# Kernel tuning notes

Hardware: AMD Instinct MI355X
Metric: run time of the kernel (lower is better)

The kernel has to match this reference:

```python
import jax, jax.numpy as jnp
import numpy as np

E, H, I, T, K = 8, 2048, 1024, 4096, 2
GROUP = 32


def dequant_int4(packed, scale, group):
    """packed: [E, R, C//2] ints in [0,256) holding two 4-bit values per byte.
    scale: [E, R, C//group]. Returns fp32 [E, R, C] with w = (nibble - 8) * scale."""
    lo = (packed & 0xF) - 8          # even columns
    hi = ((packed >> 4) & 0xF) - 8   # odd columns
    e, r, ch = packed.shape
    w = jnp.stack([lo, hi], axis=-1).reshape(e, r, 2 * ch).astype(jnp.float32)
    w = w.reshape(e, r, -1, group) * scale[..., None]
    return w.reshape(e, r, 2 * ch)


def setup_inputs() -> dict:
    key = jax.random.key(0)
    ks = jax.random.split(key, 6)
    x = jax.random.normal(ks[0], (T, H), dtype=jnp.float32)
    w1 = jax.random.randint(ks[1], (E, 2 * I, H // 2), 0, 256, dtype=jnp.int32)
    w1_scale = jax.random.uniform(ks[2], (E, 2 * I, H // GROUP), dtype=jnp.float32) * 0.02
    w2 = jax.random.randint(ks[3], (E, H, I // 2), 0, 256, dtype=jnp.int32)
    w2_scale = jax.random.uniform(ks[4], (E, H, I // GROUP), dtype=jnp.float32) * 0.02
    logits = jax.random.normal(ks[5], (T, E), dtype=jnp.float32)
    top_vals, top_idx = jax.lax.top_k(logits, K)
    expert_weights = jax.nn.softmax(top_vals, axis=-1)   # [T, K]
    expert_indices = top_idx.astype(jnp.int32)           # [T, K]
    return {"x": x, "w1": w1, "w1_scale": w1_scale, "w2": w2,
            "w2_scale": w2_scale, "expert_weights": expert_weights,
            "expert_indices": expert_indices, "top_k": K}


def reference(x, w1, w1_scale, w2, w2_scale, expert_weights, expert_indices, top_k):
    inter = w2.shape[2] * 2
    W1 = dequant_int4(w1, w1_scale, GROUP)   # [E, 2I, H]
    W2 = dequant_int4(w2, w2_scale, GROUP)   # [E, H, I]
    y13 = jnp.einsum('th,erh->etr', x, W1)   # [E, T, 2I]
    gate, up = y13[..., :inter], y13[..., inter:]
    h = jax.nn.silu(gate) * up               # [E, T, I] SwiGLU
    y = jnp.einsum('eti,ehi->eth', h, W2)    # [E, T, H]
    t_ids = jnp.arange(x.shape[0])[:, None]  # [T, 1]
    sel = y[expert_indices, t_ids, :]        # [T, K, H]
    return jnp.einsum('tkh,tk->th', sel, expert_weights)
```

## Files before the change

kernel.cpp:

```cpp
#include <hip/hip_runtime.h>
#include <cstdint>
#include <cstddef>

typedef unsigned int u32;
typedef unsigned short u16;
typedef __bf16 bf16x8 __attribute__((ext_vector_type(8)));
typedef float f32x4 __attribute__((ext_vector_type(4)));
typedef u16 u16x8 __attribute__((ext_vector_type(8)));

static constexpr int T_TOK = 4096;
static constexpr int HID   = 2048;
static constexpr int INTER = 1024;
static constexpr int NEXP  = 8;
static constexpr int TOPK  = 2;
static constexpr int SLOT_CAP = 10240;
static constexpr int NT_M = SLOT_CAP / 256;

static constexpr int META_TOK = 32;
static constexpr int META_SLOTOF = 32 + SLOT_CAP;

__device__ __forceinline__ u16 f2bf(float f) {
  u32 u = __builtin_bit_cast(u32, f);
  u32 r = (u + 0x7fffu + ((u >> 16) & 1u)) >> 16;
  return (u16)r;
}
__device__ __forceinline__ float bf2f(u16 h) {
  return __builtin_bit_cast(float, (u32)h << 16);
}

__global__ void router_count(const int* __restrict__ eidx, int* __restrict__ meta) {
  __shared__ int cnt[NEXP];
  const int tid = threadIdx.x;
  if (tid < NEXP) cnt[tid] = 0;
  __syncthreads();
  for (int i = tid; i < T_TOK * TOPK; i += 256) atomicAdd(&cnt[eidx[i]], 1);
  __syncthreads();
  if (tid == 0) {
    int off = 0;
    for (int e = 0; e < NEXP; ++e) {
      int c = cnt[e];
      meta[e] = c;
      meta[8 + e] = off;
      meta[17 + e] = off;
      off += (c + 255) & ~255;
    }
    meta[16] = off;
  }
}

__global__ void toklist_init(int* __restrict__ meta) {
  const int i = blockIdx.x * 256 + threadIdx.x;
  if (i < SLOT_CAP) meta[META_TOK + i] = 0;
}

__global__ void router_assign(const int* __restrict__ eidx, int* __restrict__ meta) {
  const int t = blockIdx.x * 256 + threadIdx.x;
  if (t >= T_TOK) return;
  int* cursors = meta + 17;
  int* toklist = meta + META_TOK;
  int* slot_of = meta + META_SLOTOF;
  for (int k = 0; k < TOPK; ++k) {
    const int e = eidx[t * TOPK + k];
    const int pos = atomicAdd(&cursors[e], 1);
    toklist[pos] = t;
    slot_of[t * TOPK + k] = pos;
  }
}

template <int CPR>
__global__ void dequant_k(const int* __restrict__ p, const float* __restrict__ s,
                          u16* __restrict__ w) {
  const int gid = blockIdx.x * 256 + threadIdx.x;
  const int row = gid / CPR;
  const int cid = gid % CPR;
  const int4 pk = *(const int4*)(p + (size_t)gid * 4);
  const float sc = s[(size_t)row * (CPR / 4) + (cid >> 2)];
  int v[4] = {pk.x, pk.y, pk.z, pk.w};
  u16x8 o;
#pragma unroll
  for (int b = 0; b < 4; ++b) {
    o[2 * b]     = f2bf((float)((v[b] & 15) - 8) * sc);
    o[2 * b + 1] = f2bf((float)(((v[b] >> 4) & 15) - 8) * sc);
  }
  *(u16x8*)(w + (size_t)gid * 8) = o;
}

__global__ void cast_x_k(const float* __restrict__ x, u16* __restrict__ xb) {
  const int i = (blockIdx.x * 256 + threadIdx.x) * 8;
  const float4 a = *(const float4*)(x + i);
  const float4 b = *(const float4*)(x + i + 4);
  u16x8 o;
  o[0] = f2bf(a.x); o[1] = f2bf(a.y); o[2] = f2bf(a.z); o[3] = f2bf(a.w);
  o[4] = f2bf(b.x); o[5] = f2bf(b.y); o[6] = f2bf(b.z); o[7] = f2bf(b.w);
  *(u16x8*)(xb + i) = o;
}

template <int KT, bool GATHER, bool GUP>
__global__ __launch_bounds__(512, 2) void gemm256(const u16* __restrict__ A,
                                                  const u16* __restrict__ B,
                                                  u16* __restrict__ Cout,
                                                  const int* __restrict__ meta) {
  static constexpr int NT = KT / 64;
  static constexpr int OSTR = GUP ? INTER : HID;

  const int bid = blockIdx.x;
  const int mt = bid % NT_M;
  const int nt = bid / NT_M;
  const int slot0 = mt * 256;
  if (slot0 >= meta[16]) return;
  int e = 0;
#pragma unroll
  for (int i = 1; i < NEXP; ++i) e += (slot0 >= meta[8 + i]);
  const int tid = threadIdx.x;

  __shared__ u16 lds[2 * 32768];
  char* ldsB = (char*)lds;

  const u16* Be = B + (size_t)e * 2048 * KT;
  const int* toklist = meta + META_TOK;

  const u16* asrc[4];
  const u16* bsrc[4];
#pragma unroll
  for (int j = 0; j < 4; ++j) {
    const int L = j * 8192 + tid * 16;
    const int S = L >> 10;
    int o = L & 1023;
    o ^= ((o >> 8) & 3) << 4;
    const int r = (S >> 1) * 16 + (o >> 6);
    const int cb = (S & 1) * 64 + (o & 63);
    const int arow = GATHER ? toklist[slot0 + r] : (slot0 + r);
    asrc[j] = A + (size_t)arow * KT + (cb >> 1);
    int brow;
    if (GUP) {
      const int g = r >> 6, j6 = r & 63;
      brow = nt * 128 + g * 32 + (j6 & 31) + ((j6 >> 5) << 10);
    } else {
      brow = nt * 256 + r;
    }
    bsrc[j] = Be + (size_t)brow * KT + (cb >> 1);
  }

#define STG_A(kt_, c_, j_)                                                          \
  __builtin_amdgcn_global_load_lds(                                                 \
      (const __attribute__((address_space(1))) void*)(asrc[j_] + (kt_) * 64),       \
      (__attribute__((address_space(3))) void*)(ldsB + (c_) * 65536 + (j_) * 8192 + \
                                                tid * 16),                           \
      16, 0, 0)
#define STG_B(kt_, c_, j_)                                                          \
  __builtin_amdgcn_global_load_lds(                                                 \
      (const __attribute__((address_space(1))) void*)(bsrc[j_] + (kt_) * 64),       \
      (__attribute__((address_space(3))) void*)(ldsB + (c_) * 65536 + 32768 +       \
                                                (j_) * 8192 + tid * 16),             \
      16, 0, 0)

  const int lane = tid & 63;
  const int wid = tid >> 6;
  const int wm = (wid >> 2) * 128;
  const int wn = (wid & 3) * 64;
  const int fr = lane & 15;
  const int qq = lane >> 4;
  const int swz = (qq * 16) ^ (((fr >> 2) & 3) << 4);

  const int abase = (wm >> 4) * 2048 + fr * 64 + swz;
  const int bbase = 32768 + (wn >> 4) * 2048 + fr * 64 + swz;

  f32x4 acc[8][4];
#pragma unroll
  for (int m = 0; m < 8; ++m)
#pragma unroll
    for (int n = 0; n < 4; ++n) acc[m][n] = (f32x4)0.0f;

  bf16x8 af[4][2], b01[2][2], b23[2][2];

#define BARRIER asm volatile("s_barrier" ::: "memory")
#define LGKM0                                              \
  do {                                                     \
    asm volatile("s_waitcnt lgkmcnt(0)" ::: "memory");     \
    __builtin_amdgcn_sched_barrier(0);                     \
  } while (0)

#define DS_AF(c_, mh_)                                                              \
  _Pragma("unroll") for (int mf = 0; mf < 4; ++mf)                                  \
  _Pragma("unroll") for (int ks = 0; ks < 2; ++ks)                                  \
      af[mf][ks] = *(const bf16x8*)(ldsB + (c_) * 65536 + abase + (mh_) * 8192 +    \
                                    mf * 2048 + ks * 1024);
#define DS_B(c_, bh_, BV_)                                                          \
  _Pragma("unroll") for (int nf = 0; nf < 2; ++nf)                                  \
  _Pragma("unroll") for (int ks = 0; ks < 2; ++ks)                                  \
      BV_[nf][ks] = *(const bf16x8*)(ldsB + (c_) * 65536 + bbase +                  \
                                     ((bh_) * 2 + nf) * 2048 + ks * 1024);
#define MFMA16(mh_, bh_, BV_)                                                       \
  do {                                                                              \
    __builtin_amdgcn_s_setprio(1);                                                  \
    _Pragma("unroll") for (int mf = 0; mf < 4; ++mf)                                \
    _Pragma("unroll") for (int nf = 0; nf < 2; ++nf)                                \
    _Pragma("unroll") for (int ks = 0; ks < 2; ++ks)                                \
        acc[(mh_) * 4 + mf][(bh_) * 2 + nf] =                                       \
            __builtin_amdgcn_mfma_f32_16x16x32_bf16(                                \
                af[mf][ks], BV_[nf][ks], acc[(mh_) * 4 + mf][(bh_) * 2 + nf],       \
                0, 0, 0);                                                           \
    __builtin_amdgcn_s_setprio(0);                                                  \
  } while (0)

  STG_A(0, 0, 0); STG_A(0, 0, 2); STG_B(0, 0, 0); STG_B(0, 0, 1);
  STG_B(0, 0, 2); STG_B(0, 0, 3); STG_A(0, 0, 1); STG_A(0, 0, 3);
  STG_A(1, 1, 0); STG_A(1, 1, 2); STG_B(1, 1, 0); STG_B(1, 1, 1);
  STG_B(1, 1, 2); STG_B(1, 1, 3); STG_A(1, 1, 1); STG_A(1, 1, 3);
  asm volatile("s_waitcnt vmcnt(8)" ::: "memory");
  BARRIER;

#pragma unroll 1
  for (int it = 0; it < NT / 2; ++it) {
    const int s0 = (2 * it + 2) & (NT - 1);
    const int s1 = (2 * it + 3) & (NT - 1);
    DS_AF(0, 0); DS_B(0, 0, b01);
    BARRIER; LGKM0; MFMA16(0, 0, b01); BARRIER;
    DS_B(0, 1, b23); STG_A(s0, 0, 0); STG_A(s0, 0, 2);
    BARRIER; LGKM0; MFMA16(0, 1, b23); BARRIER;
    DS_AF(0, 1); STG_B(s0, 0, 0); STG_B(s0, 0, 1);
    BARRIER; LGKM0; MFMA16(1, 0, b01); BARRIER;
    STG_B(s0, 0, 2); STG_B(s0, 0, 3);
    BARRIER; MFMA16(1, 1, b23);
    asm volatile("s_waitcnt vmcnt(6)" ::: "memory");
    BARRIER;
    DS_AF(1, 0); DS_B(1, 0, b01); STG_A(s0, 0, 1); STG_A(s0, 0, 3);
    BARRIER; LGKM0; MFMA16(0, 0, b01); BARRIER;
    DS_B(1, 1, b23); STG_A(s1, 1, 0); STG_A(s1, 1, 2);
    BARRIER; LGKM0; MFMA16(0, 1, b23); BARRIER;
    DS_AF(1, 1); STG_B(s1, 1, 0); STG_B(s1, 1, 1); STG_B(s1, 1, 2); STG_B(s1, 1, 3);
    BARRIER; LGKM0; MFMA16(1, 0, b01); BARRIER;
    STG_A(s1, 1, 1); STG_A(s1, 1, 3);
    BARRIER; MFMA16(1, 1, b23);
    asm volatile("s_waitcnt vmcnt(8)" ::: "memory");
    BARRIER;
  }
#undef STG_A
#undef STG_B
#undef BARRIER
#undef LGKM0
#undef DS_AF
#undef DS_B
#undef MFMA16

  if (GUP) {
    const int g = wid & 3;
#pragma unroll
    for (int mi = 0; mi < 8; ++mi)
#pragma unroll
      for (int n = 0; n < 2; ++n)
#pragma unroll
        for (int jj = 0; jj < 4; ++jj) {
          const float gv = acc[mi][n][jj];
          const float uv = acc[mi][n + 2][jj];
          const float hv = gv / (1.0f + __expf(-gv)) * uv;
          const int row = slot0 + wm + mi * 16 + qq * 4 + jj;
          Cout[(size_t)row * OSTR + nt * 128 + g * 32 + n * 16 + fr] = f2bf(hv);
        }
  } else {
#pragma unroll
    for (int mi = 0; mi < 8; ++mi)
#pragma unroll
      for (int n = 0; n < 4; ++n)
#pragma unroll
        for (int jj = 0; jj < 4; ++jj) {
          const int row = slot0 + wm + mi * 16 + qq * 4 + jj;
          const int col = nt * 256 + wn + n * 16 + fr;
          Cout[(size_t)row * OSTR + col] = f2bf(acc[mi][n][jj]);
        }
  }
}

__global__ void combine_k(const u16* __restrict__ yp, const float* __restrict__ ew,
                          const int* __restrict__ meta, float* __restrict__ out) {
  const int idx = blockIdx.x * 256 + threadIdx.x;
  const int t = idx >> 8;
  const int pos = (idx & 255) * 8;
  const int* slot_of = meta + META_SLOTOF;
  const int s0 = slot_of[t * 2];
  const int s1 = slot_of[t * 2 + 1];
  const float w0 = ew[t * 2];
  const float w1 = ew[t * 2 + 1];
  const u16x8 v0 = *(const u16x8*)(yp + (size_t)s0 * 2048 + pos);
  const u16x8 v1 = *(const u16x8*)(yp + (size_t)s1 * 2048 + pos);
  float* dst = out + (size_t)t * 2048 + pos;
  float4 o0, o1;
  o0.x = w0 * bf2f(v0[0]) + w1 * bf2f(v1[0]);
  o0.y = w0 * bf2f(v0[1]) + w1 * bf2f(v1[1]);
  o0.z = w0 * bf2f(v0[2]) + w1 * bf2f(v1[2]);
  o0.w = w0 * bf2f(v0[3]) + w1 * bf2f(v1[3]);
  o1.x = w0 * bf2f(v0[4]) + w1 * bf2f(v1[4]);
  o1.y = w0 * bf2f(v0[5]) + w1 * bf2f(v1[5]);
  o1.z = w0 * bf2f(v0[6]) + w1 * bf2f(v1[6]);
  o1.w = w0 * bf2f(v0[7]) + w1 * bf2f(v1[7]);
  *(float4*)dst = o0;
  *(float4*)(dst + 4) = o1;
}

extern "C" void kernel_launch(void* const* d_in, const int* in_sizes, int n_in,
                              void* d_out, int out_size, void* d_ws, size_t ws_size,
                              hipStream_t stream) {
  const float* x    = (const float*)d_in[0];
  const int*   w1   = (const int*)d_in[1];
  const float* w1s  = (const float*)d_in[2];
  const int*   w2   = (const int*)d_in[3];
  const float* w2s  = (const float*)d_in[4];
  const float* ew   = (const float*)d_in[5];
  const int*   eidx = (const int*)d_in[6];
  float* out = (float*)d_out;

  char* ws = (char*)d_ws;
  const size_t OFF_W1B  = 0;
  const size_t OFF_W2B  = 67108864;
  const size_t OFF_XB   = 100663296;
  const size_t OFF_H    = 117440512;
  const size_t OFF_META = 138412032;
  const size_t NEED     = 138485888;
  if (ws_size < NEED) return;

  u16* W1b  = (u16*)(ws + OFF_W1B);
  u16* yp   = (u16*)(ws + OFF_W1B);
  u16* W2b  = (u16*)(ws + OFF_W2B);
  u16* xb   = (u16*)(ws + OFF_XB);
  u16* hbuf = (u16*)(ws + OFF_H);
  int* meta = (int*)(ws + OFF_META);

  router_count<<<1, 256, 0, stream>>>(eidx, meta);
  toklist_init<<<SLOT_CAP / 256, 256, 0, stream>>>(meta);
  router_assign<<<T_TOK / 256, 256, 0, stream>>>(eidx, meta);

  cast_x_k<<<(T_TOK * HID) / (256 * 8), 256, 0, stream>>>(x, xb);
  dequant_k<256><<<16384 * 256 / 256, 256, 0, stream>>>(w1, w1s, W1b);
  dequant_k<128><<<16384 * 128 / 256, 256, 0, stream>>>(w2, w2s, W2b);

  gemm256<2048, true, true><<<NT_M * 8, 512, 0, stream>>>(xb, W1b, hbuf, meta);
  gemm256<1024, false, false><<<NT_M * 8, 512, 0, stream>>>(hbuf, W2b, yp, meta);

  combine_k<<<(T_TOK * HID) / (256 * 8), 256, 0, stream>>>(yp, ew, meta, out);
}
```

Baseline: 288.6 us.

## Fuse cast, dequant and both GEMMs into one persistent work-queue kernel

Replaces the separate cast, dequant, two GEMM and combine launches with a single persistent kernel. Blocks pull items from an atomic queue and wait on per-expert and per-tile counters, so dequant of later experts and GEMM work can overlap. The combine step moves into the second GEMM epilogue as fp32 atomicAdd into a pre-zeroed output, which removes the bf16 intermediate y buffer. The LDS swizzle pattern also changes. In exchange it adds spin-wait dependencies that rely on queue ordering, atomic contention on the output, and non-deterministic summation order.

```diff
diff --git a/kernel.cpp b/kernel.cpp
--- a/kernel.cpp
+++ b/kernel.cpp
@@ -14,10 +14,22 @@
 static constexpr int NEXP  = 8;
 static constexpr int TOPK  = 2;
 static constexpr int SLOT_CAP = 10240;
-static constexpr int NT_M = SLOT_CAP / 256;
-
-static constexpr int META_TOK = 32;
-static constexpr int META_SLOTOF = 32 + SLOT_CAP;
+static constexpr int NT_M = 40;
+
+static constexpr int M_TOT  = 16;
+static constexpr int M_CUR  = 17;
+static constexpr int M_Q    = 25;
+static constexpr int M_CAST = 26;
+static constexpr int M_ZERO = 27;
+static constexpr int M_W2   = 28;
+static constexpr int M_W1   = 29;
+static constexpr int M_DONE = 40;
+static constexpr int M_TOK  = 96;
+static constexpr int M_INTS = 96 + SLOT_CAP;
+
+static constexpr int N_CAST = 32, N_ZERO = 32, N_W2 = 64, N_W1 = 128, N_G = 320;
+static constexpr int IT_ZERO0 = 32, IT_W20 = 64, IT_W10 = 128, IT_G10 = 256,
+                     IT_G20 = 576, N_ITEMS = 896;
 
 __device__ __forceinline__ u16 f2bf(float f) {
   u32 u = __builtin_bit_cast(u32, f);
@@ -26,6 +38,18 @@
 }
 __device__ __forceinline__ float bf2f(u16 h) {
   return __builtin_bit_cast(float, (u32)h << 16);
+}
+
+__device__ __forceinline__ void spin_ge(int* p, int target) {
+  while (__hip_atomic_load(p, __ATOMIC_ACQUIRE, __HIP_MEMORY_SCOPE_AGENT) < target)
+    __builtin_amdgcn_s_sleep(8);
+}
+__device__ __forceinline__ void bump(int* p, int tid) {
+  __syncthreads();
+  if (tid == 0) {
+    __threadfence();
+    __hip_atomic_fetch_add(p, 1, __ATOMIC_RELEASE, __HIP_MEMORY_SCOPE_AGENT);
+  }
 }
 
 __global__ void router_count(const int* __restrict__ eidx, int* __restrict__ meta) {
@@ -41,36 +65,41 @@
       int c = cnt[e];
       meta[e] = c;
       meta[8 + e] = off;
-      meta[17 + e] = off;
+      meta[M_CUR + e] = off;
       off += (c + 255) & ~255;
     }
-    meta[16] = off;
-  }
-}
-
-__global__ void toklist_init(int* __restrict__ meta) {
+    meta[M_TOT] = off;
+  }
+}
+
+__global__ void init_k(int* __restrict__ meta) {
   const int i = blockIdx.x * 256 + threadIdx.x;
-  if (i < SLOT_CAP) meta[META_TOK + i] = 0;
-}
-
-__global__ void router_assign(const int* __restrict__ eidx, int* __restrict__ meta) {
+  float* ewslot = (float*)(meta + M_INTS);
+  if (i < SLOT_CAP) {
+    meta[M_TOK + i] = 0;
+    ewslot[i] = 0.0f;
+  }
+  if (blockIdx.x == 0 && threadIdx.x < 71) meta[M_Q + threadIdx.x] = 0;
+}
+
+__global__ void router_assign(const int* __restrict__ eidx, const float* __restrict__ ew,
+                              int* __restrict__ meta) {
   const int t = blockIdx.x * 256 + threadIdx.x;
   if (t >= T_TOK) return;
-  int* cursors = meta + 17;
-  int* toklist = meta + META_TOK;
-  int* slot_of = meta + META_SLOTOF;
+  int* cursors = meta + M_CUR;
+  int* toklist = meta + M_TOK;
+  float* ewslot = (float*)(meta + M_INTS);
   for (int k = 0; k < TOPK; ++k) {
     const int e = eidx[t * TOPK + k];
     const int pos = atomicAdd(&cursors[e], 1);
     toklist[pos] = t;
-    slot_of[t * TOPK + k] = pos;
+    ewslot[pos] = ew[t * TOPK + k];
   }
 }
 
 template <int CPR>
-__global__ void dequant_k(const int* __restrict__ p, const float* __restrict__ s,
-                          u16* __restrict__ w) {
-  const int gid = blockIdx.x * 256 + threadIdx.x;
+__device__ __forceinline__ void deq1(const int* __restrict__ p, const float* __restrict__ s,
+                                     u16* __restrict__ w, int gid) {
   const int row = gid / CPR;
   const int cid = gid % CPR;
   const int4 pk = *(const int4*)(p + (size_t)gid * 4);
@@ -85,39 +114,14 @@
   *(u16x8*)(w + (size_t)gid * 8) = o;
 }
 
-__global__ void cast_x_k(const float* __restrict__ x, u16* __restrict__ xb) {
-  const int i = (blockIdx.x * 256 + threadIdx.x) * 8;
-  const float4 a = *(const float4*)(x + i);
-  const float4 b = *(const float4*)(x + i + 4);
-  u16x8 o;
-  o[0] = f2bf(a.x); o[1] = f2bf(a.y); o[2] = f2bf(a.z); o[3] = f2bf(a.w);
-  o[4] = f2bf(b.x); o[5] = f2bf(b.y); o[6] = f2bf(b.z); o[7] = f2bf(b.w);
-  *(u16x8*)(xb + i) = o;
-}
-
-template <int KT, bool GATHER, bool GUP>
-__global__ __launch_bounds__(512, 2) void gemm256(const u16* __restrict__ A,
-                                                  const u16* __restrict__ B,
-                                                  u16* __restrict__ Cout,
-                                                  const int* __restrict__ meta) {
+template <int KT, bool GUP>
+__device__ void gemm_body(const u16* __restrict__ A, const u16* __restrict__ Be,
+                          u16* __restrict__ hb, float* __restrict__ out,
+                          const int* __restrict__ toklist, const float* __restrict__ ewslot,
+                          u16* lds, int slot0, int nt, int tid) {
   static constexpr int NT = KT / 64;
   static constexpr int OSTR = GUP ? INTER : HID;
-
-  const int bid = blockIdx.x;
-  const int mt = bid % NT_M;
-  const int nt = bid / NT_M;
-  const int slot0 = mt * 256;
-  if (slot0 >= meta[16]) return;
-  int e = 0;
-#pragma unroll
-  for (int i = 1; i < NEXP; ++i) e += (slot0 >= meta[8 + i]);
-  const int tid = threadIdx.x;
-
-  __shared__ u16 lds[2 * 32768];
   char* ldsB = (char*)lds;
-
-  const u16* Be = B + (size_t)e * 2048 * KT;
-  const int* toklist = meta + META_TOK;
 
   const u16* asrc[4];
   const u16* bsrc[4];
@@ -126,10 +130,10 @@
     const int L = j * 8192 + tid * 16;
     const int S = L >> 10;
     int o = L & 1023;
-    o ^= ((o >> 8) & 3) << 4;
+    o ^= ((o >> 7) & 3) << 4;
     const int r = (S >> 1) * 16 + (o >> 6);
     const int cb = (S & 1) * 64 + (o & 63);
-    const int arow = GATHER ? toklist[slot0 + r] : (slot0 + r);
+    const int arow = GUP ? toklist[slot0 + r] : (slot0 + r);
     asrc[j] = A + (size_t)arow * KT + (cb >> 1);
     int brow;
     if (GUP) {
@@ -160,7 +164,7 @@
   const int wn = (wid & 3) * 64;
   const int fr = lane & 15;
   const int qq = lane >> 4;
-  const int swz = (qq * 16) ^ (((fr >> 2) & 3) << 4);
+  const int swz = (qq * 16) ^ (((fr >> 1) & 3) << 4);
 
   const int abase = (wm >> 4) * 2048 + fr * 64 + swz;
   const int bbase = 32768 + (wn >> 4) * 2048 + fr * 64 + swz;
@@ -179,7 +183,6 @@
     asm volatile("s_waitcnt lgkmcnt(0)" ::: "memory");     \
     __builtin_amdgcn_sched_barrier(0);                     \
   } while (0)
-
 #define DS_AF(c_, mh_)                                                              \
   _Pragma("unroll") for (int mf = 0; mf < 4; ++mf)                                  \
   _Pragma("unroll") for (int ks = 0; ks < 2; ++ks)                                  \
@@ -255,46 +258,104 @@
           const float uv = acc[mi][n + 2][jj];
           const float hv = gv / (1.0f + __expf(-gv)) * uv;
           const int row = slot0 + wm + mi * 16 + qq * 4 + jj;
-          Cout[(size_t)row * OSTR + nt * 128 + g * 32 + n * 16 + fr] = f2bf(hv);
+          hb[(size_t)row * OSTR + nt * 128 + g * 32 + n * 16 + fr] = f2bf(hv);
         }
   } else {
 #pragma unroll
     for (int mi = 0; mi < 8; ++mi)
 #pragma unroll
-      for (int n = 0; n < 4; ++n)
-#pragma unroll
-        for (int jj = 0; jj < 4; ++jj) {
-          const int row = slot0 + wm + mi * 16 + qq * 4 + jj;
-          const int col = nt * 256 + wn + n * 16 + fr;
-          Cout[(size_t)row * OSTR + col] = f2bf(acc[mi][n][jj]);
+      for (int jj = 0; jj < 4; ++jj) {
+        const int slot = slot0 + wm + mi * 16 + qq * 4 + jj;
+        const int tok = toklist[slot];
+        const float w = ewslot[slot];
+        float* orow = out + (size_t)tok * HID + nt * 256 + wn + fr;
+#pragma unroll
+        for (int n = 0; n < 4; ++n)
+          atomicAdd(orow + n * 16, w * acc[mi][n][jj]);
+      }
+  }
+}
+
+__global__ __launch_bounds__(512, 2) void fused(
+    const float* __restrict__ x, const int* __restrict__ w1,
+    const float* __restrict__ w1s, const int* __restrict__ w2,
+    const float* __restrict__ w2s, u16* __restrict__ xb, u16* __restrict__ W1b,
+    u16* __restrict__ W2b, u16* __restrict__ hbuf, float* __restrict__ out,
+    int* __restrict__ meta) {
+  __shared__ u16 lds[2 * 32768];
+  __shared__ int sh_item;
+  const int tid = threadIdx.x;
+  const int* toklist = meta + M_TOK;
+  const float* ewslot = (const float*)(meta + M_INTS);
+
+  for (;;) {
+    __syncthreads();
+    if (tid == 0) sh_item = atomicAdd(&meta[M_Q], 1);
+    __syncthreads();
+    const int item = sh_item;
+    if (item >= N_ITEMS) return;
+
+    if (item < IT_ZERO0) {
+      const int base = item * 262144;
+      for (int i2 = 0; i2 < 64; ++i2) {
+        const int i = base + i2 * 4096 + tid * 8;
+        const float4 a = *(const float4*)(x + i);
+        const float4 b = *(const float4*)(x + i + 4);
+        u16x8 o;
+        o[0] = f2bf(a.x); o[1] = f2bf(a.y); o[2] = f2bf(a.z); o[3] = f2bf(a.w);
+        o[4] = f2bf(b.x); o[5] = f2bf(b.y); o[6] = f2bf(b.z); o[7] = f2bf(b.w);
+        *(u16x8*)(xb + i) = o;
+      }
+      bump(&meta[M_CAST], tid);
+    } else if (item < IT_W20) {
+      const int base = (item - IT_ZERO0) * 262144;
+      const float4 z = {0.f, 0.f, 0.f, 0.f};
+      for (int i2 = 0; i2 < 128; ++i2)
+        *(float4*)(out + base + i2 * 2048 + tid * 4) = z;
+      bump(&meta[M_ZERO], tid);
+    } else if (item < IT_W10) {
+      const int g0 = (item - IT_W20) * 32768;
+      for (int i2 = 0; i2 < 64; ++i2) deq1<128>(w2, w2s, W2b, g0 + i2 * 512 + tid);
+      bump(&meta[M_W2], tid);
+    } else if (item < IT_G10) {
+      const int iw = item - IT_W10;
+      const int g0 = iw * 32768;
+      for (int i2 = 0; i2 < 64; ++i2) deq1<256>(w1, w1s, W1b, g0 + i2 * 512 + tid);
+      bump(&meta[M_W1 + (iw >> 4)], tid);
+    } else if (item < IT_G20) {
+      const int t = item - IT_G10, mt = t >> 3, nt = t & 7;
+      const int slot0 = mt * 256;
+      if (slot0 < meta[M_TOT]) {
+        int e = 0;
+#pragma unroll
+        for (int i = 1; i < NEXP; ++i) e += (slot0 >= meta[8 + i]);
+        if (tid == 0) {
+          spin_ge(&meta[M_CAST], N_CAST);
+          spin_ge(&meta[M_W1 + e], 16);
         }
-  }
-}
-
-__global__ void combine_k(const u16* __restrict__ yp, const float* __restrict__ ew,
-                          const int* __restrict__ meta, float* __restrict__ out) {
-  const int idx = blockIdx.x * 256 + threadIdx.x;
-  const int t = idx >> 8;
-  const int pos = (idx & 255) * 8;
-  const int* slot_of = meta + META_SLOTOF;
-  const int s0 = slot_of[t * 2];
-  const int s1 = slot_of[t * 2 + 1];
-  const float w0 = ew[t * 2];
-  const float w1 = ew[t * 2 + 1];
-  const u16x8 v0 = *(const u16x8*)(yp + (size_t)s0 * 2048 + pos);
-  const u16x8 v1 = *(const u16x8*)(yp + (size_t)s1 * 2048 + pos);
-  float* dst = out + (size_t)t * 2048 + pos;
-  float4 o0, o1;
-  o0.x = w0 * bf2f(v0[0]) + w1 * bf2f(v1[0]);
-  o0.y = w0 * bf2f(v0[1]) + w1 * bf2f(v1[1]);
-  o0.z = w0 * bf2f(v0[2]) + w1 * bf2f(v1[2]);
-  o0.w = w0 * bf2f(v0[3]) + w1 * bf2f(v1[3]);
-  o1.x = w0 * bf2f(v0[4]) + w1 * bf2f(v1[4]);
-  o1.y = w0 * bf2f(v0[5]) + w1 * bf2f(v1[5]);
-  o1.z = w0 * bf2f(v0[6]) + w1 * bf2f(v1[6]);
-  o1.w = w0 * bf2f(v0[7]) + w1 * bf2f(v1[7]);
-  *(float4*)dst = o0;
-  *(float4*)(dst + 4) = o1;
+        __syncthreads();
+        gemm_body<2048, true>(xb, W1b + (size_t)e * 2048 * 2048, hbuf, out,
+                              toklist, ewslot, lds, slot0, nt, tid);
+        bump(&meta[M_DONE + mt], tid);
+      }
+    } else {
+      const int t = item - IT_G20, mt = t >> 3, nt = t & 7;
+      const int slot0 = mt * 256;
+      if (slot0 < meta[M_TOT]) {
+        int e = 0;
+#pragma unroll
+        for (int i = 1; i < NEXP; ++i) e += (slot0 >= meta[8 + i]);
+        if (tid == 0) {
+          spin_ge(&meta[M_ZERO], N_ZERO);
+          spin_ge(&meta[M_W2], N_W2);
+          spin_ge(&meta[M_DONE + mt], 8);
+        }
+        __syncthreads();
+        gemm_body<1024, false>(hbuf, W2b + (size_t)e * 2048 * 1024, hbuf, out,
+                               toklist, ewslot, lds, slot0, nt, tid);
+      }
+    }
+  }
 }
 
 extern "C" void kernel_launch(void* const* d_in, const int* in_sizes, int n_in,
@@ -315,26 +376,18 @@
   const size_t OFF_XB   = 100663296;
   const size_t OFF_H    = 117440512;
   const size_t OFF_META = 138412032;
-  const size_t NEED     = 138485888;
+  const size_t NEED     = 138494336;
   if (ws_size < NEED) return;
 
   u16* W1b  = (u16*)(ws + OFF_W1B);
-  u16* yp   = (u16*)(ws + OFF_W1B);
   u16* W2b  = (u16*)(ws + OFF_W2B);
   u16* xb   = (u16*)(ws + OFF_XB);
   u16* hbuf = (u16*)(ws + OFF_H);
   int* meta = (int*)(ws + OFF_META);
 
   router_count<<<1, 256, 0, stream>>>(eidx, meta);
-  toklist_init<<<SLOT_CAP / 256, 256, 0, stream>>>(meta);
-  router_assign<<<T_TOK / 256, 256, 0, stream>>>(eidx, meta);
-
-  cast_x_k<<<(T_TOK * HID) / (256 * 8), 256, 0, stream>>>(x, xb);
-  dequant_k<256><<<16384 * 256 / 256, 256, 0, stream>>>(w1, w1s, W1b);
-  dequant_k<128><<<16384 * 128 / 256, 256, 0, stream>>>(w2, w2s, W2b);
-
-  gemm256<2048, true, true><<<NT_M * 8, 512, 0, stream>>>(xb, W1b, hbuf, meta);
-  gemm256<1024, false, false><<<NT_M * 8, 512, 0, stream>>>(hbuf, W2b, yp, meta);
-
-  combine_k<<<(T_TOK * HID) / (256 * 8), 256, 0, stream>>>(yp, ew, meta, out);
-}
+  init_k<<<SLOT_CAP / 256, 256, 0, stream>>>(meta);
+  router_assign<<<T_TOK / 256, 256, 0, stream>>>(eidx, ew, meta);
+
+  fused<<<256, 512, 0, stream>>>(x, w1, w1s, w2, w2s, xb, W1b, W2b, hbuf, out, meta);
+}
```

Measured after the change: 486.9 us. 68.7% more time.
